# Optimization experiments

Hardware: AMD Instinct MI355X
Metric: run time of the kernel (lower is better)

## Reference

```python
import jax, jax.numpy as jnp
import numpy as np

KERNEL = 7
DS_LIM = 0.01
ALPHA_M = 1.0


def _smooth_field(field):
    # field [3,D,H,W] -> depthwise mean filter with kernel 7, SAME padding
    k = KERNEL
    w = jnp.ones((3, 1, k, k, k), dtype=field.dtype) / (k ** 3)
    out = jax.lax.conv_general_dilated(
        field[None], w, (1, 1, 1), 'SAME',
        dimension_numbers=('NCDHW', 'OIDHW', 'NCDHW'),
        feature_group_count=3)
    return out[0]


def _trilinear(vol, coords):
    # vol [B,D,H,W]; coords [B,3,D,H,W] in voxel units
    B, D, H, W = vol.shape
    cz = jnp.clip(coords[:, 0], 0.0, D - 1.0)
    cy = jnp.clip(coords[:, 1], 0.0, H - 1.0)
    cx = jnp.clip(coords[:, 2], 0.0, W - 1.0)
    z0 = jnp.floor(cz).astype(jnp.int32); z1 = jnp.minimum(z0 + 1, D - 1)
    y0 = jnp.floor(cy).astype(jnp.int32); y1 = jnp.minimum(y0 + 1, H - 1)
    x0 = jnp.floor(cx).astype(jnp.int32); x1 = jnp.minimum(x0 + 1, W - 1)
    fz = cz - z0; fy = cy - y0; fx = cx - x0
    b = jnp.arange(B)[:, None, None, None]
    g = lambda zi, yi, xi: vol[b, zi, yi, xi]
    c00 = g(z0, y0, x0) * (1 - fx) + g(z0, y0, x1) * fx
    c01 = g(z0, y1, x0) * (1 - fx) + g(z0, y1, x1) * fx
    c10 = g(z1, y0, x0) * (1 - fx) + g(z1, y0, x1) * fx
    c11 = g(z1, y1, x0) * (1 - fx) + g(z1, y1, x1) * fx
    c0 = c00 * (1 - fy) + c01 * fy
    c1 = c10 * (1 - fy) + c11 * fy
    return c0 * (1 - fz) + c1 * fz


def setup_inputs() -> dict:
    key = jax.random.key(0)
    ks = jax.random.split(key, 8)
    B, C, L = 8, 128, 5
    D = H = W = 96
    return {
        'encode_ds': jax.random.normal(ks[0], (B, C, L, L, L), jnp.float32),
        'orig': jax.random.normal(ks[1], (B, 1, D, H, W), jnp.float32),
        'mask': jax.random.uniform(ks[2], (B, 1, D, H, W), jnp.float32),
        'c1_w': jax.random.normal(ks[3], (1, C, 1, 1, 1), jnp.float32) * 0.05,
        'c1_b': jnp.zeros((1,), jnp.float32),
        'f1_w': jax.random.normal(ks[4], (1, L ** 3), jnp.float32) * 0.1,
        'f1_b': jnp.zeros((1,), jnp.float32),
        'offset_field': jax.random.normal(ks[5], (3, D, H, W), jnp.float32),
    }


def reference(encode_ds, orig, mask, c1_w, c1_b, f1_w, f1_b, offset_field):
    B = encode_ds.shape[0]
    # 1x1x1 Conv3d (128 -> 1) is a per-voxel channel contraction
    a = jnp.einsum('bcdhw,c->bdhw', encode_ds, c1_w[0, :, 0, 0, 0]) + c1_b[0]
    a = a.reshape(B, -1)                                   # [B, 125]
    alpha = jax.nn.sigmoid(a @ f1_w[0] + f1_b[0]) * ALPHA_M  # [B]

    # deform: smoothed, ds_lim-clamped offset field scaled by per-sample alpha
    field = jnp.clip(_smooth_field(offset_field), -DS_LIM, DS_LIM)  # [3,D,H,W]
    _, _, D, H, W = orig.shape
    base = jnp.stack(jnp.meshgrid(jnp.arange(D, dtype=orig.dtype),
                                  jnp.arange(H, dtype=orig.dtype),
                                  jnp.arange(W, dtype=orig.dtype),
                                  indexing='ij'))          # [3,D,H,W]
    scale = jnp.array([D, H, W], orig.dtype).reshape(1, 3, 1, 1, 1)
    disp = alpha[:, None, None, None, None] * field[None] * scale  # [B,3,D,H,W]
    coords = base[None] + disp

    def_ = _trilinear(orig[:, 0], coords)[:, None]
    mask_d = _trilinear(mask[:, 0], coords)[:, None]
    return def_, mask_d
```

## Files before the change

kernel.cpp:

```cpp
#include <hip/hip_runtime.h>
#include <hip/hip_fp16.h>
#include <math.h>

#define DD 96
#define VOX (96*96*96)
#define NB 8
#define NC 128
#define L3 125

#define BTZ 8
#define BTS 16
#define NBZ 12
#define NBY 6
#define NBX 6
#define BNTILE (NBZ*NBY*NBX)
#define BHZ 14
#define BHY 22
#define XROW 225
#define XSN (BHY * XROW)

#define TZ 12
#define TY 8
#define TX 32
#define NTZ 8
#define NTY 12
#define NTX 3
#define STILE (NTZ*NTY*NTX)
#define HZS 14
#define HYS 10
#define HXS 34
#define HXP 35
#define HLDS (HZS*HYS*HXP)
#define NPAIR (HZS*HYS*17)

typedef float vfloat2 __attribute__((ext_vector_type(2)));
typedef float vfloat4 __attribute__((ext_vector_type(4)));
typedef float f2u __attribute__((ext_vector_type(2), aligned(4)));

static __device__ __forceinline__ vfloat2 h2f(__half2 h) {
    float2 t = __half22float2(h);
    vfloat2 r; r.x = t.x; r.y = t.y;
    return r;
}

__global__ __launch_bounds__(256, 8) void blur_alpha(
        const float* __restrict__ in, float* __restrict__ out,
        const float* __restrict__ enc,
        const float* __restrict__ c1_w, const float* __restrict__ c1_b,
        const float* __restrict__ f1_w, const float* __restrict__ f1_b,
        float* __restrict__ alpha) {
    __shared__ float xs[XSN];
    __shared__ float red[4];
    int tid = threadIdx.x;

    if (blockIdx.x >= 3 * BNTILE) {
        int b = blockIdx.x - 3 * BNTILE;
        const float4* e4 = (const float4*)(enc + (size_t)b * NC * L3);
        float s = 0.f;
        for (int j = tid; j < (NC * L3) / 4; j += 256) {
            float4 v = e4[j];
            int f = j * 4;
            s += v.x * c1_w[(f + 0) / L3] * f1_w[(f + 0) % L3];
            s += v.y * c1_w[(f + 1) / L3] * f1_w[(f + 1) % L3];
            s += v.z * c1_w[(f + 2) / L3] * f1_w[(f + 2) % L3];
            s += v.w * c1_w[(f + 3) / L3] * f1_w[(f + 3) % L3];
        }
        for (int off = 32; off > 0; off >>= 1) s += __shfl_down(s, off, 64);
        int lane = tid & 63, wid = tid >> 6;
        if (lane == 0) red[wid] = s;
        __syncthreads();
        if (tid == 0) {
            float tot = red[0] + red[1] + red[2] + red[3];
            float fwsum = 0.f;
            for (int v = 0; v < L3; ++v) fwsum += f1_w[v];
            float x = tot + c1_b[0] * fwsum + f1_b[0];
            alpha[b] = 1.f / (1.f + expf(-x));
        }
        return;
    }

    int blk = blockIdx.x;
    int c = blk / BNTILE;
    int t = blk % BNTILE;
    int tz = t / (NBY * NBX), ty = (t / NBX) % NBY, tx = t % NBX;
    int bz = tz * BTZ, by = ty * BTS, bx = tx * BTS;
    const float* ib = in + (size_t)c * VOX;

    for (int u = tid; u < 2 * BHY * BHZ; u += 256) {
        int half = (u >= BHY * BHZ) ? 1 : 0;
        int rr = u - half * (BHY * BHZ);
        int hy = rr / BHZ, hz = rr - (rr / BHZ) * BHZ;
        int gz = bz + hz - 3, gy = by + hy - 3;
        float* xrow = &xs[hy * XROW + hz * 16 + half * 8];
        if ((unsigned)gz >= DD || (unsigned)gy >= DD) {
            #pragma unroll
            for (int xo = 0; xo < 8; ++xo) xrow[xo] = 0.f;
            continue;
        }
        const float* rp = ib + (gz * DD + gy) * DD;
        int x0 = bx + half * 8;
        int base = x0 - 4;
        if (base < 0) base = 0;
        if (base > DD - 16) base = DD - 16;
        const float4* p4 = (const float4*)(rp + base);
        float w[16];
        #pragma unroll
        for (int q = 0; q < 4; ++q) {
            float4 t4 = p4[q];
            w[q * 4 + 0] = t4.x; w[q * 4 + 1] = t4.y;
            w[q * 4 + 2] = t4.z; w[q * 4 + 3] = t4.w;
        }
        float v[14];
        if (x0 == 0) {
            v[0] = v[1] = v[2] = 0.f;
            #pragma unroll
            for (int j = 3; j < 14; ++j) v[j] = w[j - 3];
        } else if (x0 == DD - 8) {
            #pragma unroll
            for (int j = 0; j < 11; ++j) v[j] = w[j + 5];
            v[11] = v[12] = v[13] = 0.f;
        } else {
            #pragma unroll
            for (int j = 0; j < 14; ++j) v[j] = w[j + 1];
        }
        float s = v[0] + v[1] + v[2] + v[3] + v[4] + v[5] + v[6];
        xrow[0] = s;
        #pragma unroll
        for (int xo = 1; xo < 8; ++xo) {
            s += v[xo + 6] - v[xo - 1];
            xrow[xo] = s;
        }
    }
    __syncthreads();

    if (tid < BHZ * BTS) {
        int hz = tid >> 4, xo = tid & 15;
        int base = hz * 16 + xo;
        float s = 0.f;
        #pragma unroll
        for (int hy = 0; hy < 7; ++hy) s += xs[hy * XROW + base];
        #pragma unroll
        for (int yo = 0; yo < 16; ++yo) {
            float old = xs[yo * XROW + base];
            float nxt = (yo < 15) ? xs[(yo + 7) * XROW + base] : 0.f;
            xs[yo * XROW + base] = s;
            s += nxt - old;
        }
    }
    __syncthreads();

    {
        int yo = tid >> 4, xo = tid & 15;
        int base = yo * XROW + xo;
        float s = 0.f;
        #pragma unroll
        for (int hz = 0; hz < 7; ++hz) s += xs[base + hz * 16];
        float* ob = out + (size_t)c * VOX + (by + yo) * DD + bx + xo;
        #pragma unroll
        for (int zo = 0; zo < BTZ; ++zo) {
            float v = s * (1.0f / 343.0f);
            v = fminf(fmaxf(v, -0.01f), 0.01f) * 96.0f;
            ob[(size_t)(bz + zo) * DD * DD] = v;
            s += xs[base + (zo + 7) * 16] - xs[base + zo * 16];
        }
    }
}

__global__ __launch_bounds__(256, 8) void sample_tile(
        const float* __restrict__ orig,
        const float* __restrict__ mask,
        const float* __restrict__ field,
        const float* __restrict__ alpha,
        float* __restrict__ out) {
    __shared__ __half2 tile[HLDS];

    int blk = blockIdx.x;
    int b = blk / STILE;
    int r = blk % STILE;
    int o = r & 7;
    int l = r >> 3;
    int zh = o >> 2;
    int yq = o & 3;
    int lz4 = l / 9, ly3 = (l / 3) % 3, lx3 = l % 3;
    int tz = zh * 4 + lz4;
    int ty = yq * 3 + ly3;
    int tx = lx3;
    int bz = tz * TZ, by = ty * TY, bx = tx * TX;

    const float* ob = orig + (size_t)b * VOX;
    const float* mb = mask + (size_t)b * VOX;
    int tid = threadIdx.x;

    for (int u = tid; u < NPAIR; u += 256) {
        int row = u / 17, p = u - row * 17;
        int hz = row / HYS, hy = row - (row / HYS) * HYS;
        int gz = min(max(bz + hz - 1, 0), DD - 1);
        int gy = min(max(by + hy - 1, 0), DD - 1);
        int gx0 = bx - 1 + 2 * p;
        int base = min(max(gx0, 0), DD - 2);
        int g = (gz * DD + gy) * DD + base;
        f2u o2 = *(const f2u*)(ob + g);
        f2u m2 = *(const f2u*)(mb + g);
        float oa = (gx0 > DD - 2) ? o2.y : o2.x;
        float obv = (gx0 < 0) ? o2.x : o2.y;
        float ma = (gx0 > DD - 2) ? m2.y : m2.x;
        float mbv = (gx0 < 0) ? m2.x : m2.y;
        int idx = (hz * HYS + hy) * HXP + 2 * p;
        tile[idx]     = __floats2half2_rn(oa, ma);
        tile[idx + 1] = __floats2half2_rn(obv, mbv);
    }
    float a = alpha[b];
    __syncthreads();

    const vfloat4* fz4 = (const vfloat4*)field;
    const vfloat4* fy4 = (const vfloat4*)(field + VOX);
    const vfloat4* fx4 = (const vfloat4*)(field + 2 * VOX);
    vfloat4* oD = (vfloat4*)(out);
    vfloat4* oM = (vfloat4*)(out + (size_t)NB * VOX);

    int lz  = tid >> 6;
    int ly  = (tid >> 3) & 7;
    int lxq = tid & 7;
    int gy  = by + ly;
    int gx0 = bx + 4 * lxq;
    float gyf = (float)gy;
    float gx0f = (float)gx0;
    float c1z = (float)(1 - bz), c1y = (float)(1 - by), c1x = (float)(1 - bx);

    auto samp = [&](float gzf, float dzv, float dyv, float dxv,
                    float gxf) -> vfloat2 {
        float cz = fminf(fmaxf(fmaf(a, dzv, gzf), 0.f), (float)(DD - 1)) + c1z;
        float cy = fminf(fmaxf(fmaf(a, dyv, gyf), 0.f), (float)(DD - 1)) + c1y;
        float cx = fminf(fmaxf(fmaf(a, dxv, gxf), 0.f), (float)(DD - 1)) + c1x;
        float flz = floorf(cz), fly = floorf(cy), flx = floorf(cx);
        float fzf = cz - flz, fyf = cy - fly, fxf = cx - flx;
        int iz = (int)flz, iy = (int)fly, ix = (int)flx;

        const __half2* tp = tile + (iz * HYS + iy) * HXP + ix;
        vfloat2 v000 = h2f(tp[0]);
        vfloat2 v001 = h2f(tp[1]);
        vfloat2 v010 = h2f(tp[HXP]);
        vfloat2 v011 = h2f(tp[HXP + 1]);
        vfloat2 v100 = h2f(tp[HYS * HXP]);
        vfloat2 v101 = h2f(tp[HYS * HXP + 1]);
        vfloat2 v110 = h2f(tp[(HYS + 1) * HXP]);
        vfloat2 v111 = h2f(tp[(HYS + 1) * HXP + 1]);

        vfloat2 FX = {fxf, fxf}, FY = {fyf, fyf}, FZ = {fzf, fzf};
        vfloat2 c00 = v000 + FX * (v001 - v000);
        vfloat2 c01 = v010 + FX * (v011 - v010);
        vfloat2 c10 = v100 + FX * (v101 - v100);
        vfloat2 c11 = v110 + FX * (v111 - v110);
        vfloat2 c0 = c00 + FY * (c01 - c00);
        vfloat2 c1 = c10 + FY * (c11 - c10);
        return c0 + FZ * (c1 - c0);
    };

    int vp4 = (((bz + lz) * DD + gy) * DD + gx0) >> 2;
    vfloat4 dz = fz4[vp4], dy = fy4[vp4], dx = fx4[vp4];
    size_t ob0 = (size_t)b * (VOX / 4);

    #pragma unroll
    for (int it = 0; it < TZ / 4; ++it) {
        vfloat4 dzn = {0,0,0,0}, dyn = {0,0,0,0}, dxn = {0,0,0,0};
        if (it < TZ / 4 - 1) {
            int vq = vp4 + DD * DD;
            dzn = fz4[vq]; dyn = fy4[vq]; dxn = fx4[vq];
        }
        float gzf = (float)(bz + 4 * it + lz);

        vfloat2 r0 = samp(gzf, dz.x, dy.x, dx.x, gx0f);
        vfloat2 r1 = samp(gzf, dz.y, dy.y, dx.y, gx0f + 1.f);
        vfloat2 r2 = samp(gzf, dz.z, dy.z, dx.z, gx0f + 2.f);
        vfloat2 r3 = samp(gzf, dz.w, dy.w, dx.w, gx0f + 3.f);

        vfloat4 vD = {r0.x, r1.x, r2.x, r3.x};
        vfloat4 vM = {r0.y, r1.y, r2.y, r3.y};
        __builtin_nontemporal_store(vD, &oD[ob0 + vp4]);
        __builtin_nontemporal_store(vM, &oM[ob0 + vp4]);

        vp4 += DD * DD;
        dz = dzn; dy = dyn; dx = dxn;
    }
}

extern "C" void kernel_launch(void* const* d_in, const int* in_sizes, int n_in,
                              void* d_out, int out_size, void* d_ws, size_t ws_size,
                              hipStream_t stream) {
    const float* enc   = (const float*)d_in[0];
    const float* orig  = (const float*)d_in[1];
    const float* mask  = (const float*)d_in[2];
    const float* c1_w  = (const float*)d_in[3];
    const float* c1_b  = (const float*)d_in[4];
    const float* f1_w  = (const float*)d_in[5];
    const float* f1_b  = (const float*)d_in[6];
    const float* offs  = (const float*)d_in[7];
    float* out = (float*)d_out;

    float* ws = (float*)d_ws;
    float* alpha = ws;
    float* fieldB = ws + 16;

    blur_alpha<<<3 * BNTILE + NB, 256, 0, stream>>>(
        offs, fieldB, enc, c1_w, c1_b, f1_w, f1_b, alpha);
    sample_tile<<<NB * STILE, 256, 0, stream>>>(orig, mask, fieldB, alpha, out);
}
```

Measured before the change: 167.1 us.

## Enlarge sampling tile Y extent and remap threads to two-voxel rows

```diff
diff --git a/kernel.cpp b/kernel.cpp
--- a/kernel.cpp
+++ b/kernel.cpp
@@ -20,16 +20,15 @@
 #define XSN (BHY * XROW)
 
 #define TZ 12
-#define TY 8
+#define TY 12
 #define TX 32
 #define NTZ 8
-#define NTY 12
+#define NTY 8
 #define NTX 3
 #define STILE (NTZ*NTY*NTX)
 #define HZS 14
-#define HYS 10
-#define HXS 34
-#define HXP 35
+#define HYS 14
+#define HXP 34
 #define HLDS (HZS*HYS*HXP)
 #define NPAIR (HZS*HYS*17)
 
@@ -43,7 +42,7 @@
     return r;
 }
 
-__global__ __launch_bounds__(256, 8) void blur_alpha(
+__global__ __launch_bounds__(256, 6) void blur_alpha(
         const float* __restrict__ in, float* __restrict__ out,
         const float* __restrict__ enc,
         const float* __restrict__ c1_w, const float* __restrict__ c1_b,
@@ -166,7 +165,7 @@
     }
 }
 
-__global__ __launch_bounds__(256, 8) void sample_tile(
+__global__ __launch_bounds__(256, 6) void sample_tile(
         const float* __restrict__ orig,
         const float* __restrict__ mask,
         const float* __restrict__ field,
@@ -181,9 +180,11 @@
     int l = r >> 3;
     int zh = o >> 2;
     int yq = o & 3;
-    int lz4 = l / 9, ly3 = (l / 3) % 3, lx3 = l % 3;
+    int lz4 = l / 6;
+    int rem = l - lz4 * 6;
+    int ly2 = rem / 3, lx3 = rem - ly2 * 3;
     int tz = zh * 4 + lz4;
-    int ty = yq * 3 + ly3;
+    int ty = yq * 2 + ly2;
     int tx = lx3;
     int bz = tz * TZ, by = ty * TY, bx = tx * TX;
 
@@ -212,23 +213,20 @@
     float a = alpha[b];
     __syncthreads();
 
-    const vfloat4* fz4 = (const vfloat4*)field;
-    const vfloat4* fy4 = (const vfloat4*)(field + VOX);
-    const vfloat4* fx4 = (const vfloat4*)(field + 2 * VOX);
-    vfloat4* oD = (vfloat4*)(out);
-    vfloat4* oM = (vfloat4*)(out + (size_t)NB * VOX);
-
-    int lz  = tid >> 6;
-    int ly  = (tid >> 3) & 7;
-    int lxq = tid & 7;
-    int gy  = by + ly;
-    int gx0 = bx + 4 * lxq;
-    float gyf = (float)gy;
+    const float2* fz2 = (const float2*)field;
+    const float2* fy2 = (const float2*)(field + VOX);
+    const float2* fx2 = (const float2*)(field + 2 * VOX);
+    vfloat2* oD = (vfloat2*)(out);
+    vfloat2* oM = (vfloat2*)(out + (size_t)NB * VOX);
+
+    int px  = tid & 15;
+    int r0  = tid >> 4;
+    int gx0 = bx + 2 * px;
     float gx0f = (float)gx0;
     float c1z = (float)(1 - bz), c1y = (float)(1 - by), c1x = (float)(1 - bx);
 
-    auto samp = [&](float gzf, float dzv, float dyv, float dxv,
-                    float gxf) -> vfloat2 {
+    auto samp = [&](float gzf, float gyf, float gxf, float dzv, float dyv,
+                    float dxv) -> vfloat2 {
         float cz = fminf(fmaxf(fmaf(a, dzv, gzf), 0.f), (float)(DD - 1)) + c1z;
         float cy = fminf(fmaxf(fmaf(a, dyv, gyf), 0.f), (float)(DD - 1)) + c1y;
         float cx = fminf(fmaxf(fmaf(a, dxv, gxf), 0.f), (float)(DD - 1)) + c1x;
@@ -256,31 +254,26 @@
         return c0 + FZ * (c1 - c0);
     };
 
-    int vp4 = (((bz + lz) * DD + gy) * DD + gx0) >> 2;
-    vfloat4 dz = fz4[vp4], dy = fy4[vp4], dx = fx4[vp4];
-    size_t ob0 = (size_t)b * (VOX / 4);
-
-    #pragma unroll
-    for (int it = 0; it < TZ / 4; ++it) {
-        vfloat4 dzn = {0,0,0,0}, dyn = {0,0,0,0}, dxn = {0,0,0,0};
-        if (it < TZ / 4 - 1) {
-            int vq = vp4 + DD * DD;
-            dzn = fz4[vq]; dyn = fy4[vq]; dxn = fx4[vq];
-        }
-        float gzf = (float)(bz + 4 * it + lz);
-
-        vfloat2 r0 = samp(gzf, dz.x, dy.x, dx.x, gx0f);
-        vfloat2 r1 = samp(gzf, dz.y, dy.y, dx.y, gx0f + 1.f);
-        vfloat2 r2 = samp(gzf, dz.z, dy.z, dx.z, gx0f + 2.f);
-        vfloat2 r3 = samp(gzf, dz.w, dy.w, dx.w, gx0f + 3.f);
-
-        vfloat4 vD = {r0.x, r1.x, r2.x, r3.x};
-        vfloat4 vM = {r0.y, r1.y, r2.y, r3.y};
-        __builtin_nontemporal_store(vD, &oD[ob0 + vp4]);
-        __builtin_nontemporal_store(vM, &oM[ob0 + vp4]);
-
-        vp4 += DD * DD;
-        dz = dzn; dy = dyn; dx = dxn;
+    size_t ob0 = (size_t)b * (VOX / 2);
+
+    #pragma unroll 3
+    for (int k = 0; k < 9; ++k) {
+        int row = r0 + k * 16;
+        int z = row / 12;
+        int y = row - z * 12;
+        int gz = bz + z, gy = by + y;
+        int vp2 = ((gz * DD + gy) * DD + gx0) >> 1;
+
+        float2 dz = fz2[vp2], dy = fy2[vp2], dx = fx2[vp2];
+        float gzf = (float)gz, gyf = (float)gy;
+
+        vfloat2 s0 = samp(gzf, gyf, gx0f,       dz.x, dy.x, dx.x);
+        vfloat2 s1 = samp(gzf, gyf, gx0f + 1.f, dz.y, dy.y, dx.y);
+
+        vfloat2 vD = {s0.x, s1.x};
+        vfloat2 vM = {s0.y, s1.y};
+        __builtin_nontemporal_store(vD, &oD[ob0 + vp2]);
+        __builtin_nontemporal_store(vM, &oM[ob0 + vp2]);
     }
 }
 
```

After: 156.8 us. 1.07x faster.
